# Optimization experiments

Hardware: AMD Instinct MI355X
Metric: run time of the kernel (lower is better)

The kernel has to match this reference:

```python
import jax, jax.numpy as jnp
import numpy as np

N, E, G = 50000, 800000, 500
IN_DIM, EXTRA, HID, HEADS, NCLS = 128, 32, 64, 4, 1
NODE_FEAT2 = HID * HEADS  # 256, input to layer 2
FINAL = NODE_FEAT2 + EXTRA
NODES_PER_GRAPH = N // G  # 100


def gat_layer(h, W, a_l, a_r, b, src, dst, internal_relu):
    # DGL GATConv: fc -> per-head attn logits -> leaky_relu -> edge softmax (over dst) -> weighted sum
    feat = (h @ W).reshape(N, HEADS, HID)            # [N,H,D]
    el = jnp.sum(feat * a_l, axis=-1)                # [N,H]
    er = jnp.sum(feat * a_r, axis=-1)                # [N,H]
    e = jax.nn.leaky_relu(el[src] + er[dst], negative_slope=0.2)  # [E,H]
    m = jax.ops.segment_max(e, dst, num_segments=N)  # [N,H] (stable softmax)
    ex = jnp.exp(e - m[dst])
    denom = jax.ops.segment_sum(ex, dst, num_segments=N)
    alpha = ex / denom[dst]                          # [E,H]
    msg = feat[src] * alpha[:, :, None]              # [E,H,D]
    rst = jax.ops.segment_sum(msg, dst, num_segments=N) + b.reshape(1, HEADS, HID)
    if internal_relu:
        rst = jax.nn.relu(rst)
    return rst


def setup_inputs() -> dict:
    key = jax.random.key(0)
    ks = jax.random.split(key, 20)
    s = 0.05
    inp = {
        "x": jax.random.normal(ks[0], (N, IN_DIM), jnp.float32),
        "desc": jax.random.normal(ks[1], (G, EXTRA), jnp.float32),
        "src": jax.random.randint(ks[2], (E,), 0, N, jnp.int32),
        "dst": jax.random.randint(ks[3], (E,), 0, N, jnp.int32),
        "graph_id": (jnp.arange(N) // NODES_PER_GRAPH).astype(jnp.int32),
        # layer 1 params
        "W1": jax.random.normal(ks[4], (IN_DIM, HEADS * HID), jnp.float32) * s,
        "al1": jax.random.normal(ks[5], (HEADS, HID), jnp.float32) * s,
        "ar1": jax.random.normal(ks[6], (HEADS, HID), jnp.float32) * s,
        "b1": jnp.zeros((HEADS * HID,), jnp.float32),
        # layer 2 params
        "W2": jax.random.normal(ks[7], (NODE_FEAT2, HEADS * HID), jnp.float32) * s,
        "al2": jax.random.normal(ks[8], (HEADS, HID), jnp.float32) * s,
        "ar2": jax.random.normal(ks[9], (HEADS, HID), jnp.float32) * s,
        "b2": jnp.zeros((HEADS * HID,), jnp.float32),
        # MLP head (weights stored [in,out])
        "fc1_w": jax.random.normal(ks[10], (FINAL, HID), jnp.float32) * s,
        "fc1_b": jnp.zeros((HID,), jnp.float32),
        "fc2_w": jax.random.normal(ks[11], (HID, HID // 2), jnp.float32) * s,
        "fc2_b": jnp.zeros((HID // 2,), jnp.float32),
        "out_w": jax.random.normal(ks[12], (HID // 2, NCLS), jnp.float32) * s,
        "out_b": jnp.zeros((NCLS,), jnp.float32),
    }
    return inp


def reference(x, desc, src, dst, graph_id, W1, al1, ar1, b1, W2, al2, ar2, b2,
              fc1_w, fc1_b, fc2_w, fc2_b, out_w, out_b):
    h = gat_layer(x, W1, al1, ar1, b1, src, dst, internal_relu=True)
    h = jax.nn.relu(h.reshape(N, -1))                # flatten heads + outer relu (dropout=0)
    h = gat_layer(h, W2, al2, ar2, b2, src, dst, internal_relu=False)
    h = jax.nn.relu(h.reshape(N, -1))
    # dgl.mean_nodes over batched graph
    hg = jax.ops.segment_sum(h, graph_id, num_segments=G) / float(NODES_PER_GRAPH)  # [G, 256]
    combined = jnp.concatenate([hg, desc], axis=1)   # [G, 288]
    z = jax.nn.relu(combined @ fc1_w + fc1_b)
    z = jax.nn.relu(z @ fc2_w + fc2_b)
    return z @ out_w + out_b                          # [G, 1]
```

## Files before the change

### kernel.cpp

```cpp
#include <hip/hip_runtime.h>
#include <hip/hip_bf16.h>

#define N_NODES 50000
#define N_EDGES 800000
#define N_GRAPHS 500
#define IN_DIM 128
#define EXTRA 32
#define HID 64
#define HEADS 4
#define F2 256
#define NODES_PER_GRAPH 100
#define SCAN_BLOCKS ((N_NODES + 1023) / 1024)

typedef unsigned short u16;
typedef __attribute__((ext_vector_type(8))) short short8;
typedef __attribute__((ext_vector_type(4))) float floatx4;

__device__ __forceinline__ float bf2f(u16 u) {
    union { unsigned int i; float f; } v;
    v.i = ((unsigned int)u) << 16;
    return v.f;
}
__device__ __forceinline__ u16 f2b(float f) {
    __hip_bfloat16 h = __float2bfloat16(f);
    return *reinterpret_cast<u16*>(&h);
}

#define CNT_BLK 3125
#define CVT_BLK 6250
#define RP1_BLK 16
#define RP2_BLK 32
__global__ __launch_bounds__(256) void prep_kernel(const int* __restrict__ dst,
                                                   int* __restrict__ cnt,
                                                   const float* __restrict__ x,
                                                   u16* __restrict__ xb,
                                                   const float* __restrict__ W1,
                                                   u16* __restrict__ BF1,
                                                   const float* __restrict__ W2,
                                                   u16* __restrict__ BF2) {
    int b = blockIdx.x, t = threadIdx.x;
    if (b < CNT_BLK) {
        int e = b * 256 + t;
        if (e < N_EDGES) atomicAdd(&cnt[dst[e]], 1);
    } else if (b < CNT_BLK + CVT_BLK) {
        int i = (b - CNT_BLK) * 256 + t;
        float4 v = reinterpret_cast<const float4*>(x)[i];
        ushort4 o;
        o.x = f2b(v.x); o.y = f2b(v.y); o.z = f2b(v.z); o.w = f2b(v.w);
        reinterpret_cast<ushort4*>(xb)[i] = o;
    } else {
        const float* W;
        u16* BF;
        int chunk;
        if (b < CNT_BLK + CVT_BLK + RP1_BLK) {
            W = W1; BF = BF1; chunk = (b - CNT_BLK - CVT_BLK) * 4 + (t >> 6);
        } else {
            W = W2; BF = BF2; chunk = (b - CNT_BLK - CVT_BLK - RP1_BLK) * 4 + (t >> 6);
        }
        int l = t & 63;
        int kt = chunk >> 4, ct = chunk & 15;
        int col = ct * 16 + (l & 15);
        int k0 = kt * 32 + 8 * (l >> 4);
        u16* p = BF + (size_t)chunk * 512 + l * 8;
#pragma unroll
        for (int j = 0; j < 8; ++j) p[j] = f2b(W[(size_t)(k0 + j) * 256 + col]);
    }
}

__global__ __launch_bounds__(1024) void scan_block_kernel(const int* __restrict__ cnt,
                                                          int* __restrict__ part,
                                                          int* __restrict__ bsum) {
    __shared__ int buf[1024];
    int b = blockIdx.x, t = threadIdx.x;
    int i = b * 1024 + t;
    buf[t] = (i < N_NODES) ? cnt[i] : 0;
    __syncthreads();
    for (int d = 1; d < 1024; d <<= 1) {
        int add = (t >= d) ? buf[t - d] : 0;
        __syncthreads();
        buf[t] += add;
        __syncthreads();
    }
    if (i < N_NODES) part[i] = buf[t];
    if (t == 1023) bsum[b] = buf[t];
}

__global__ __launch_bounds__(1024) void scan_finalize_kernel(const int* __restrict__ part,
                                                             const int* __restrict__ bsum,
                                                             int* __restrict__ offs) {
    __shared__ int sbase;
    int t = threadIdx.x;
    if (t < 64) {
        int v = (t < blockIdx.x) ? bsum[t] : 0;
#pragma unroll
        for (int d = 32; d > 0; d >>= 1) v += __shfl_xor(v, d);
        if (t == 0) sbase = v;
    }
    __syncthreads();
    int i = blockIdx.x * 1024 + t;
    if (i < N_NODES) {
        offs[i + 1] = part[i] + sbase;
        if (i == 0) offs[0] = 0;
    }
}

__global__ void scatter_kernel(const int* __restrict__ src, const int* __restrict__ dst,
                               const int* __restrict__ offs, int* __restrict__ fill,
                               int* __restrict__ csr_src, int* __restrict__ pos_arr) {
    int e = blockIdx.x * blockDim.x + threadIdx.x;
    if (e < N_EDGES) {
        int d = dst[e];
        int pos = offs[d] + atomicAdd(&fill[d], 1);
        csr_src[pos] = src[e];
        pos_arr[e] = pos;
    }
}

__global__ void edge_w_kernel(const int* __restrict__ src, const int* __restrict__ dst,
                              const int* __restrict__ pos_arr,
                              const float* __restrict__ el, const float* __restrict__ er,
                              float* __restrict__ w) {
    int e = blockIdx.x * blockDim.x + threadIdx.x;
    if (e >= N_EDGES) return;
    int s = src[e], d = dst[e], p = pos_arr[e];
    float4 l = *reinterpret_cast<const float4*>(&el[s * 4]);
    float4 r = *reinterpret_cast<const float4*>(&er[d * 4]);
    float4 o; float v;
    v = l.x + r.x; v = (v > 0.f) ? v : 0.2f * v; o.x = __expf(v);
    v = l.y + r.y; v = (v > 0.f) ? v : 0.2f * v; o.y = __expf(v);
    v = l.z + r.z; v = (v > 0.f) ? v : 0.2f * v; o.z = __expf(v);
    v = l.w + r.w; v = (v > 0.f) ? v : 0.2f * v; o.w = __expf(v);
    *reinterpret_cast<float4*>(&w[(size_t)p * 4]) = o;
}

template <int K>
__global__ __launch_bounds__(256) void gemm_mfma_attn_kernel(const u16* __restrict__ A,
                                                             const u16* __restrict__ BF,
                                                             const float* __restrict__ al,
                                                             const float* __restrict__ ar,
                                                             u16* __restrict__ C,
                                                             float* __restrict__ el,
                                                             float* __restrict__ er, int M) {
    __shared__ u16 bstage[8192];
    __shared__ u16 cxpose[4][16 * 68];
    int t = threadIdx.x;
    int wave = t >> 6, lane = t & 63;
    int wr = wave >> 1, wc = wave & 1;
    int l15 = lane & 15, kg = lane >> 4;
    int cb = blockIdx.y;
    int row0 = blockIdx.x * 128 + wr * 64;
    int h = cb * 2 + wc;
    int ct0 = cb * 8 + wc * 4;

    floatx4 acc[4][4];
#pragma unroll
    for (int s = 0; s < 4; ++s)
#pragma unroll
        for (int c = 0; c < 4; ++c) acc[s][c] = (floatx4)0.0f;

    int arow[4];
#pragma unroll
    for (int s = 0; s < 4; ++s) {
        int r = row0 + s * 16 + l15;
        arow[s] = (r < M) ? r : 0;
    }

    int schunk = t >> 4;
    int soff = (t & 15) * 32;

    for (int ks = 0; ks < K / 64; ++ks) {
        __syncthreads();
        {
            int gchunk = (ks * 2 + (schunk >> 3)) * 16 + cb * 8 + (schunk & 7);
            const u16* gp = BF + (size_t)gchunk * 512 + soff;
            u16* lp = bstage + schunk * 512 + soff;
#pragma unroll
            for (int u = 0; u < 4; ++u)
                *reinterpret_cast<short8*>(lp + u * 8) =
                    *reinterpret_cast<const short8*>(gp + u * 8);
        }
        __syncthreads();
#pragma unroll
        for (int ktl = 0; ktl < 2; ++ktl) {
            int kk = (ks * 2 + ktl) * 32 + kg * 8;
            short8 a[4], b[4];
#pragma unroll
            for (int s = 0; s < 4; ++s)
                a[s] = *reinterpret_cast<const short8*>(A + (size_t)arow[s] * K + kk);
#pragma unroll
            for (int c = 0; c < 4; ++c)
                b[c] = *reinterpret_cast<const short8*>(
                           bstage + (ktl * 8 + wc * 4 + c) * 512 + lane * 8);
#pragma unroll
            for (int s = 0; s < 4; ++s)
#pragma unroll
                for (int c = 0; c < 4; ++c)
                    acc[s][c] = __builtin_amdgcn_mfma_f32_16x16x32_bf16(a[s], b[c], acc[s][c], 0, 0, 0);
        }
    }

    floatx4 pls[4], prs[4];
#pragma unroll
    for (int s = 0; s < 4; ++s) { pls[s] = (floatx4)0.0f; prs[s] = (floatx4)0.0f; }
#pragma unroll
    for (int c = 0; c < 4; ++c) {
        float wl = al[(ct0 + c) * 16 + l15];
        float wrr = ar[(ct0 + c) * 16 + l15];
#pragma unroll
        for (int s = 0; s < 4; ++s) {
            pls[s] += acc[s][c] * wl;
            prs[s] += acc[s][c] * wrr;
        }
    }
#pragma unroll
    for (int off = 1; off < 16; off <<= 1) {
#pragma unroll
        for (int s = 0; s < 4; ++s)
#pragma unroll
            for (int j = 0; j < 4; ++j) {
                pls[s][j] += __shfl_xor(pls[s][j], off);
                prs[s][j] += __shfl_xor(prs[s][j], off);
            }
    }
    if (l15 == 0) {
#pragma unroll
        for (int s = 0; s < 4; ++s)
#pragma unroll
            for (int j = 0; j < 4; ++j) {
                int n = row0 + s * 16 + kg * 4 + j;
                if (n < M) { el[n * 4 + h] = pls[s][j]; er[n * 4 + h] = prs[s][j]; }
            }
    }

    u16* cbuf = cxpose[wave];
#pragma unroll
    for (int s = 0; s < 4; ++s) {
#pragma unroll
        for (int c = 0; c < 4; ++c)
#pragma unroll
            for (int j = 0; j < 4; ++j)
                cbuf[(kg * 4 + j) * 68 + c * 16 + l15] = f2b(acc[s][c][j]);
#pragma unroll
        for (int it = 0; it < 2; ++it) {
            int r = (lane >> 3) + it * 8;
            int cg = lane & 7;
            int grow = row0 + s * 16 + r;
            if (grow < M) {
                short8 v = *reinterpret_cast<const short8*>(cbuf + r * 68 + cg * 8);
                *reinterpret_cast<short8*>(C + (size_t)grow * 256 + ct0 * 16 + cg * 8) = v;
            }
        }
    }
}

__global__ __launch_bounds__(256) void gather_kernel(const u16* __restrict__ feat,
                                                     const float* __restrict__ w,
                                                     const int* __restrict__ offs,
                                                     const int* __restrict__ csr_src,
                                                     const float* __restrict__ bias,
                                                     u16* __restrict__ outb) {
    int n = blockIdx.x * 4 + (threadIdx.x >> 6);
    if (n >= N_NODES) return;
    int lane = threadIdx.x & 63;
    int h = lane >> 4;
    const ushort4* feat4 = reinterpret_cast<const ushort4*>(feat);
    int s0 = offs[n], s1 = offs[n + 1];
    float4 acc = make_float4(0.f, 0.f, 0.f, 0.f);
    float den = 0.f;
    int i = s0;
    for (; i + 4 <= s1; i += 4) {
        int n0 = csr_src[i], n1 = csr_src[i + 1], n2 = csr_src[i + 2], n3 = csr_src[i + 3];
        float x0 = w[(size_t)(i + 0) * 4 + h];
        float x1 = w[(size_t)(i + 1) * 4 + h];
        float x2 = w[(size_t)(i + 2) * 4 + h];
        float x3 = w[(size_t)(i + 3) * 4 + h];
        ushort4 f0 = feat4[(size_t)n0 * 64 + lane];
        ushort4 f1 = feat4[(size_t)n1 * 64 + lane];
        ushort4 f2 = feat4[(size_t)n2 * 64 + lane];
        ushort4 f3 = feat4[(size_t)n3 * 64 + lane];
        acc.x = fmaf(x0, bf2f(f0.x), acc.x); acc.y = fmaf(x0, bf2f(f0.y), acc.y);
        acc.z = fmaf(x0, bf2f(f0.z), acc.z); acc.w = fmaf(x0, bf2f(f0.w), acc.w);
        acc.x = fmaf(x1, bf2f(f1.x), acc.x); acc.y = fmaf(x1, bf2f(f1.y), acc.y);
        acc.z = fmaf(x1, bf2f(f1.z), acc.z); acc.w = fmaf(x1, bf2f(f1.w), acc.w);
        acc.x = fmaf(x2, bf2f(f2.x), acc.x); acc.y = fmaf(x2, bf2f(f2.y), acc.y);
        acc.z = fmaf(x2, bf2f(f2.z), acc.z); acc.w = fmaf(x2, bf2f(f2.w), acc.w);
        acc.x = fmaf(x3, bf2f(f3.x), acc.x); acc.y = fmaf(x3, bf2f(f3.y), acc.y);
        acc.z = fmaf(x3, bf2f(f3.z), acc.z); acc.w = fmaf(x3, bf2f(f3.w), acc.w);
        den += (x0 + x1) + (x2 + x3);
    }
    for (; i < s1; ++i) {
        int s = csr_src[i];
        float x = w[(size_t)i * 4 + h];
        ushort4 f = feat4[(size_t)s * 64 + lane];
        acc.x = fmaf(x, bf2f(f.x), acc.x); acc.y = fmaf(x, bf2f(f.y), acc.y);
        acc.z = fmaf(x, bf2f(f.z), acc.z); acc.w = fmaf(x, bf2f(f.w), acc.w);
        den += x;
    }
    float inv = (s1 > s0) ? 1.f / den : 0.f;
    float4 bv = reinterpret_cast<const float4*>(bias)[lane];
    ushort4 o;
    o.x = f2b(fmaxf(fmaf(acc.x, inv, bv.x), 0.f));
    o.y = f2b(fmaxf(fmaf(acc.y, inv, bv.y), 0.f));
    o.z = f2b(fmaxf(fmaf(acc.z, inv, bv.z), 0.f));
    o.w = f2b(fmaxf(fmaf(acc.w, inv, bv.w), 0.f));
    reinterpret_cast<ushort4*>(outb)[(size_t)n * 64 + lane] = o;
}

__global__ __launch_bounds__(256) void head_kernel(const u16* __restrict__ h2,
                                                   const float* __restrict__ desc,
                                                   const float* __restrict__ fc1_w,
                                                   const float* __restrict__ fc1_b,
                                                   const float* __restrict__ fc2_w,
                                                   const float* __restrict__ fc2_b,
                                                   const float* __restrict__ out_w,
                                                   const float* __restrict__ out_b,
                                                   float* __restrict__ out) {
    __shared__ float comb[288];
    __shared__ float z1[64];
    __shared__ float z2[32];
    int g = blockIdx.x, t = threadIdx.x;
    const u16* base = h2 + (size_t)g * NODES_PER_GRAPH * 256;
    float s = 0.f;
    for (int i = 0; i < NODES_PER_GRAPH; ++i) s += bf2f(base[(size_t)i * 256 + t]);
    comb[t] = s * (1.f / NODES_PER_GRAPH);
    if (t < EXTRA) comb[256 + t] = desc[g * EXTRA + t];
    __syncthreads();
    if (t < 64) {
        float a = fc1_b[t];
        for (int i = 0; i < 288; ++i) a += comb[i] * fc1_w[i * 64 + t];
        z1[t] = fmaxf(a, 0.f);
    }
    __syncthreads();
    if (t < 32) {
        float a = fc2_b[t];
        for (int i = 0; i < 64; ++i) a += z1[i] * fc2_w[i * 32 + t];
        z2[t] = fmaxf(a, 0.f);
    }
    __syncthreads();
    if (t == 0) {
        float a = out_b[0];
        for (int i = 0; i < 32; ++i) a += z2[i] * out_w[i];
        out[g] = a;
    }
}

extern "C" void kernel_launch(void* const* d_in, const int* in_sizes, int n_in,
                              void* d_out, int out_size, void* d_ws, size_t ws_size,
                              hipStream_t stream) {
    const float* x     = (const float*)d_in[0];
    const float* desc  = (const float*)d_in[1];
    const int*   src   = (const int*)d_in[2];
    const int*   dst   = (const int*)d_in[3];
    const float* W1    = (const float*)d_in[5];
    const float* al1   = (const float*)d_in[6];
    const float* ar1   = (const float*)d_in[7];
    const float* b1    = (const float*)d_in[8];
    const float* W2    = (const float*)d_in[9];
    const float* al2   = (const float*)d_in[10];
    const float* ar2   = (const float*)d_in[11];
    const float* b2    = (const float*)d_in[12];
    const float* fc1_w = (const float*)d_in[13];
    const float* fc1_b = (const float*)d_in[14];
    const float* fc2_w = (const float*)d_in[15];
    const float* fc2_b = (const float*)d_in[16];
    const float* out_w = (const float*)d_in[17];
    const float* out_b = (const float*)d_in[18];
    float* out = (float*)d_out;

    char* ws = (char*)d_ws;
    size_t off = 0;
    auto alloc = [&](size_t bytes) -> void* {
        void* p = ws + off;
        off = (off + bytes + 255) & ~(size_t)255;
        return p;
    };
    u16*   xb      = (u16*)alloc((size_t)N_NODES * IN_DIM * 2);
    u16*   featb   = (u16*)alloc((size_t)N_NODES * 256 * 2);
    u16*   h1b     = (u16*)alloc((size_t)N_NODES * 256 * 2);
    u16*   h2b     = (u16*)alloc((size_t)N_NODES * 256 * 2);
    u16*   BF1     = (u16*)alloc((size_t)IN_DIM * 256 * 2);
    u16*   BF2     = (u16*)alloc((size_t)F2 * 256 * 2);
    float* el      = (float*)alloc((size_t)N_NODES * 4 * 4);
    float* er      = (float*)alloc((size_t)N_NODES * 4 * 4);
    int*   offs    = (int*)alloc((size_t)(N_NODES + 1) * 4);
    int*   cntfill = (int*)alloc((size_t)2 * N_NODES * 4);
    int*   part    = (int*)alloc((size_t)N_NODES * 4);
    int*   bsum    = (int*)alloc(64 * 4);
    int*   csr_src = (int*)alloc((size_t)N_EDGES * 4);
    int*   pos_arr = (int*)alloc((size_t)N_EDGES * 4);
    float* wbuf    = (float*)alloc((size_t)N_EDGES * 4 * 4);
    int* cnt = cntfill, *fill = cntfill + N_NODES;

    hipMemsetAsync(cntfill, 0, (size_t)2 * N_NODES * 4, stream);
    prep_kernel<<<CNT_BLK + CVT_BLK + RP1_BLK + RP2_BLK, 256, 0, stream>>>(
        dst, cnt, x, xb, W1, BF1, W2, BF2);
    scan_block_kernel<<<SCAN_BLOCKS, 1024, 0, stream>>>(cnt, part, bsum);
    scan_finalize_kernel<<<SCAN_BLOCKS, 1024, 0, stream>>>(part, bsum, offs);
    scatter_kernel<<<(N_EDGES + 255) / 256, 256, 0, stream>>>(src, dst, offs, fill,
                                                              csr_src, pos_arr);

    dim3 gg((N_NODES + 127) / 128, 2);
    int eb = (N_EDGES + 255) / 256;
    gemm_mfma_attn_kernel<IN_DIM><<<gg, 256, 0, stream>>>(xb, BF1, al1, ar1, featb, el, er, N_NODES);
    edge_w_kernel<<<eb, 256, 0, stream>>>(src, dst, pos_arr, el, er, wbuf);
    gather_kernel<<<(N_NODES + 3) / 4, 256, 0, stream>>>(featb, wbuf, offs, csr_src, b1, h1b);
    gemm_mfma_attn_kernel<F2><<<gg, 256, 0, stream>>>(h1b, BF2, al2, ar2, featb, el, er, N_NODES);
    edge_w_kernel<<<eb, 256, 0, stream>>>(src, dst, pos_arr, el, er, wbuf);
    gather_kernel<<<(N_NODES + 3) / 4, 256, 0, stream>>>(featb, wbuf, offs, csr_src, b2, h2b);
    head_kernel<<<N_GRAPHS, 256, 0, stream>>>(h2b, desc, fc1_w, fc1_b, fc2_w, fc2_b,
                                              out_w, out_b, out);
}
```

Measured before the change: 314.5 us.

## Fuse CSR scatter with layer-1 edge weights and widen gather to half-wave per node

The CSR scatter is merged with the first layer's edge-weight computation, so one edge pass writes csr_src, pos_arr and the exp-weights, and a launch plus a reread of src/dst is dropped. The gather kernel now gives each node 32 lanes that each load 8 bf16 values (16-byte loads), fitting 8 nodes per block, and unrolls by 2 with a wave-wide __any loop. The head kernel's mean reduction is split into 4 accumulators. Two half-wave nodes with different degrees now share one loop, which can leave lanes idle, and the unroll drops from 4 to 2.

```diff
diff --git a/kernel.cpp b/kernel.cpp
--- a/kernel.cpp
+++ b/kernel.cpp
@@ -104,16 +104,25 @@
     }
 }
 
-__global__ void scatter_kernel(const int* __restrict__ src, const int* __restrict__ dst,
-                               const int* __restrict__ offs, int* __restrict__ fill,
-                               int* __restrict__ csr_src, int* __restrict__ pos_arr) {
+__global__ void scatter_w_kernel(const int* __restrict__ src, const int* __restrict__ dst,
+                                 const int* __restrict__ offs, int* __restrict__ fill,
+                                 int* __restrict__ csr_src, int* __restrict__ pos_arr,
+                                 const float* __restrict__ el, const float* __restrict__ er,
+                                 float* __restrict__ w) {
     int e = blockIdx.x * blockDim.x + threadIdx.x;
-    if (e < N_EDGES) {
-        int d = dst[e];
-        int pos = offs[d] + atomicAdd(&fill[d], 1);
-        csr_src[pos] = src[e];
-        pos_arr[e] = pos;
-    }
+    if (e >= N_EDGES) return;
+    int s = src[e], d = dst[e];
+    int pos = offs[d] + atomicAdd(&fill[d], 1);
+    csr_src[pos] = s;
+    pos_arr[e] = pos;
+    float4 l = *reinterpret_cast<const float4*>(&el[s * 4]);
+    float4 r = *reinterpret_cast<const float4*>(&er[d * 4]);
+    float4 o; float v;
+    v = l.x + r.x; v = (v > 0.f) ? v : 0.2f * v; o.x = __expf(v);
+    v = l.y + r.y; v = (v > 0.f) ? v : 0.2f * v; o.y = __expf(v);
+    v = l.z + r.z; v = (v > 0.f) ? v : 0.2f * v; o.z = __expf(v);
+    v = l.w + r.w; v = (v > 0.f) ? v : 0.2f * v; o.w = __expf(v);
+    *reinterpret_cast<float4*>(&w[(size_t)pos * 4]) = o;
 }
 
 __global__ void edge_w_kernel(const int* __restrict__ src, const int* __restrict__ dst,
@@ -259,51 +268,49 @@
                                                      const int* __restrict__ csr_src,
                                                      const float* __restrict__ bias,
                                                      u16* __restrict__ outb) {
-    int n = blockIdx.x * 4 + (threadIdx.x >> 6);
-    if (n >= N_NODES) return;
-    int lane = threadIdx.x & 63;
-    int h = lane >> 4;
-    const ushort4* feat4 = reinterpret_cast<const ushort4*>(feat);
-    int s0 = offs[n], s1 = offs[n + 1];
-    float4 acc = make_float4(0.f, 0.f, 0.f, 0.f);
+    int half = threadIdx.x >> 5;
+    int n = blockIdx.x * 8 + half;
+    int l = threadIdx.x & 31;
+    int h = l >> 3;
+    bool valid = n < N_NODES;
+    int s0 = valid ? offs[n] : 0;
+    int s1 = valid ? offs[n + 1] : 0;
+
+    float acc[8] = {0.f, 0.f, 0.f, 0.f, 0.f, 0.f, 0.f, 0.f};
     float den = 0.f;
     int i = s0;
-    for (; i + 4 <= s1; i += 4) {
-        int n0 = csr_src[i], n1 = csr_src[i + 1], n2 = csr_src[i + 2], n3 = csr_src[i + 3];
-        float x0 = w[(size_t)(i + 0) * 4 + h];
-        float x1 = w[(size_t)(i + 1) * 4 + h];
-        float x2 = w[(size_t)(i + 2) * 4 + h];
-        float x3 = w[(size_t)(i + 3) * 4 + h];
-        ushort4 f0 = feat4[(size_t)n0 * 64 + lane];
-        ushort4 f1 = feat4[(size_t)n1 * 64 + lane];
-        ushort4 f2 = feat4[(size_t)n2 * 64 + lane];
-        ushort4 f3 = feat4[(size_t)n3 * 64 + lane];
-        acc.x = fmaf(x0, bf2f(f0.x), acc.x); acc.y = fmaf(x0, bf2f(f0.y), acc.y);
-        acc.z = fmaf(x0, bf2f(f0.z), acc.z); acc.w = fmaf(x0, bf2f(f0.w), acc.w);
-        acc.x = fmaf(x1, bf2f(f1.x), acc.x); acc.y = fmaf(x1, bf2f(f1.y), acc.y);
-        acc.z = fmaf(x1, bf2f(f1.z), acc.z); acc.w = fmaf(x1, bf2f(f1.w), acc.w);
-        acc.x = fmaf(x2, bf2f(f2.x), acc.x); acc.y = fmaf(x2, bf2f(f2.y), acc.y);
-        acc.z = fmaf(x2, bf2f(f2.z), acc.z); acc.w = fmaf(x2, bf2f(f2.w), acc.w);
-        acc.x = fmaf(x3, bf2f(f3.x), acc.x); acc.y = fmaf(x3, bf2f(f3.y), acc.y);
-        acc.z = fmaf(x3, bf2f(f3.z), acc.z); acc.w = fmaf(x3, bf2f(f3.w), acc.w);
-        den += (x0 + x1) + (x2 + x3);
-    }
-    for (; i < s1; ++i) {
-        int s = csr_src[i];
-        float x = w[(size_t)i * 4 + h];
-        ushort4 f = feat4[(size_t)s * 64 + lane];
-        acc.x = fmaf(x, bf2f(f.x), acc.x); acc.y = fmaf(x, bf2f(f.y), acc.y);
-        acc.z = fmaf(x, bf2f(f.z), acc.z); acc.w = fmaf(x, bf2f(f.w), acc.w);
-        den += x;
-    }
-    float inv = (s1 > s0) ? 1.f / den : 0.f;
-    float4 bv = reinterpret_cast<const float4*>(bias)[lane];
-    ushort4 o;
-    o.x = f2b(fmaxf(fmaf(acc.x, inv, bv.x), 0.f));
-    o.y = f2b(fmaxf(fmaf(acc.y, inv, bv.y), 0.f));
-    o.z = f2b(fmaxf(fmaf(acc.z, inv, bv.z), 0.f));
-    o.w = f2b(fmaxf(fmaf(acc.w, inv, bv.w), 0.f));
-    reinterpret_cast<ushort4*>(outb)[(size_t)n * 64 + lane] = o;
+    while (__any(i < s1)) {
+        bool p0 = i < s1, p1 = (i + 1) < s1;
+        float x0 = 0.f, x1 = 0.f;
+        short8 f0 = (short8)0, f1 = (short8)0;
+        if (p0) {
+            int e0 = csr_src[i];
+            x0 = w[(size_t)i * 4 + h];
+            f0 = *reinterpret_cast<const short8*>(feat + (size_t)e0 * 256 + l * 8);
+        }
+        if (p1) {
+            int e1 = csr_src[i + 1];
+            x1 = w[(size_t)(i + 1) * 4 + h];
+            f1 = *reinterpret_cast<const short8*>(feat + (size_t)e1 * 256 + l * 8);
+        }
+#pragma unroll
+        for (int j = 0; j < 8; ++j) acc[j] = fmaf(x0, bf2f((u16)f0[j]), acc[j]);
+#pragma unroll
+        for (int j = 0; j < 8; ++j) acc[j] = fmaf(x1, bf2f((u16)f1[j]), acc[j]);
+        den += x0 + x1;
+        i += 2;
+    }
+    if (valid) {
+        float inv = (s1 > s0) ? 1.f / den : 0.f;
+        float4 bv0 = reinterpret_cast<const float4*>(bias)[l * 2];
+        float4 bv1 = reinterpret_cast<const float4*>(bias)[l * 2 + 1];
+        float bb[8] = {bv0.x, bv0.y, bv0.z, bv0.w, bv1.x, bv1.y, bv1.z, bv1.w};
+        short8 o;
+#pragma unroll
+        for (int j = 0; j < 8; ++j)
+            o[j] = (short)f2b(fmaxf(fmaf(acc[j], inv, bb[j]), 0.f));
+        *reinterpret_cast<short8*>(outb + (size_t)n * 256 + l * 8) = o;
+    }
 }
 
 __global__ __launch_bounds__(256) void head_kernel(const u16* __restrict__ h2,
@@ -320,9 +327,14 @@
     __shared__ float z2[32];
     int g = blockIdx.x, t = threadIdx.x;
     const u16* base = h2 + (size_t)g * NODES_PER_GRAPH * 256;
-    float s = 0.f;
-    for (int i = 0; i < NODES_PER_GRAPH; ++i) s += bf2f(base[(size_t)i * 256 + t]);
-    comb[t] = s * (1.f / NODES_PER_GRAPH);
+    float s0 = 0.f, s1 = 0.f, s2 = 0.f, s3 = 0.f;
+    for (int i = 0; i < NODES_PER_GRAPH; i += 4) {
+        s0 += bf2f(base[(size_t)(i + 0) * 256 + t]);
+        s1 += bf2f(base[(size_t)(i + 1) * 256 + t]);
+        s2 += bf2f(base[(size_t)(i + 2) * 256 + t]);
+        s3 += bf2f(base[(size_t)(i + 3) * 256 + t]);
+    }
+    comb[t] = ((s0 + s1) + (s2 + s3)) * (1.f / NODES_PER_GRAPH);
     if (t < EXTRA) comb[256 + t] = desc[g * EXTRA + t];
     __syncthreads();
     if (t < 64) {
@@ -396,17 +408,17 @@
         dst, cnt, x, xb, W1, BF1, W2, BF2);
     scan_block_kernel<<<SCAN_BLOCKS, 1024, 0, stream>>>(cnt, part, bsum);
     scan_finalize_kernel<<<SCAN_BLOCKS, 1024, 0, stream>>>(part, bsum, offs);
-    scatter_kernel<<<(N_EDGES + 255) / 256, 256, 0, stream>>>(src, dst, offs, fill,
-                                                              csr_src, pos_arr);
 
     dim3 gg((N_NODES + 127) / 128, 2);
     int eb = (N_EDGES + 255) / 256;
+    int ngb = (N_NODES + 7) / 8;
     gemm_mfma_attn_kernel<IN_DIM><<<gg, 256, 0, stream>>>(xb, BF1, al1, ar1, featb, el, er, N_NODES);
-    edge_w_kernel<<<eb, 256, 0, stream>>>(src, dst, pos_arr, el, er, wbuf);
-    gather_kernel<<<(N_NODES + 3) / 4, 256, 0, stream>>>(featb, wbuf, offs, csr_src, b1, h1b);
+    scatter_w_kernel<<<eb, 256, 0, stream>>>(src, dst, offs, fill, csr_src, pos_arr,
+                                             el, er, wbuf);
+    gather_kernel<<<ngb, 256, 0, stream>>>(featb, wbuf, offs, csr_src, b1, h1b);
     gemm_mfma_attn_kernel<F2><<<gg, 256, 0, stream>>>(h1b, BF2, al2, ar2, featb, el, er, N_NODES);
     edge_w_kernel<<<eb, 256, 0, stream>>>(src, dst, pos_arr, el, er, wbuf);
-    gather_kernel<<<(N_NODES + 3) / 4, 256, 0, stream>>>(featb, wbuf, offs, csr_src, b2, h2b);
+    gather_kernel<<<ngb, 256, 0, stream>>>(featb, wbuf, offs, csr_src, b2, h2b);
     head_kernel<<<N_GRAPHS, 256, 0, stream>>>(h2b, desc, fc1_w, fc1_b, fc2_w, fc2_b,
                                               out_w, out_b, out);
 }
```

Measured after the change: 320.9 us. 1.02x slower.

## Fuse CSR scatter with layer-1 edge weights and restage GEMM A tile in LDS

Applied to the files above, without the earlier changes.

The CSR scatter kernel now also computes the layer-1 edge attention weights, which removes one edge pass and one kernel launch. The GEMM is retiled so each block owns 64 rows across all four heads. The A tile is staged in shared memory once and reused by all four waves instead of each wave loading it from global memory, and the full B matrix slice is staged per k-step. The head kernel's per-graph mean loop is also unrolled into four independent accumulators. In exchange the GEMM uses more shared memory per block and has fewer waves per row tile, which may lower occupancy.

```diff
diff --git a/kernel.cpp b/kernel.cpp
--- a/kernel.cpp
+++ b/kernel.cpp
@@ -104,16 +104,25 @@
     }
 }
 
-__global__ void scatter_kernel(const int* __restrict__ src, const int* __restrict__ dst,
-                               const int* __restrict__ offs, int* __restrict__ fill,
-                               int* __restrict__ csr_src, int* __restrict__ pos_arr) {
+__global__ void scatter_w_kernel(const int* __restrict__ src, const int* __restrict__ dst,
+                                 const int* __restrict__ offs, int* __restrict__ fill,
+                                 int* __restrict__ csr_src, int* __restrict__ pos_arr,
+                                 const float* __restrict__ el, const float* __restrict__ er,
+                                 float* __restrict__ w) {
     int e = blockIdx.x * blockDim.x + threadIdx.x;
-    if (e < N_EDGES) {
-        int d = dst[e];
-        int pos = offs[d] + atomicAdd(&fill[d], 1);
-        csr_src[pos] = src[e];
-        pos_arr[e] = pos;
-    }
+    if (e >= N_EDGES) return;
+    int s = src[e], d = dst[e];
+    int pos = offs[d] + atomicAdd(&fill[d], 1);
+    csr_src[pos] = s;
+    pos_arr[e] = pos;
+    float4 l = *reinterpret_cast<const float4*>(&el[s * 4]);
+    float4 r = *reinterpret_cast<const float4*>(&er[d * 4]);
+    float4 o; float v;
+    v = l.x + r.x; v = (v > 0.f) ? v : 0.2f * v; o.x = __expf(v);
+    v = l.y + r.y; v = (v > 0.f) ? v : 0.2f * v; o.y = __expf(v);
+    v = l.z + r.z; v = (v > 0.f) ? v : 0.2f * v; o.z = __expf(v);
+    v = l.w + r.w; v = (v > 0.f) ? v : 0.2f * v; o.w = __expf(v);
+    *reinterpret_cast<float4*>(&w[(size_t)pos * 4]) = o;
 }
 
 __global__ void edge_w_kernel(const int* __restrict__ src, const int* __restrict__ dst,
@@ -141,16 +150,13 @@
                                                              u16* __restrict__ C,
                                                              float* __restrict__ el,
                                                              float* __restrict__ er, int M) {
-    __shared__ u16 bstage[8192];
-    __shared__ u16 cxpose[4][16 * 68];
+    __shared__ u16 astage[64][68];
+    __shared__ u16 bstage[16384];
     int t = threadIdx.x;
     int wave = t >> 6, lane = t & 63;
-    int wr = wave >> 1, wc = wave & 1;
+    int wc = wave;
     int l15 = lane & 15, kg = lane >> 4;
-    int cb = blockIdx.y;
-    int row0 = blockIdx.x * 128 + wr * 64;
-    int h = cb * 2 + wc;
-    int ct0 = cb * 8 + wc * 4;
+    int row0 = blockIdx.x * 64;
 
     floatx4 acc[4][4];
 #pragma unroll
@@ -158,39 +164,38 @@
 #pragma unroll
         for (int c = 0; c < 4; ++c) acc[s][c] = (floatx4)0.0f;
 
-    int arow[4];
-#pragma unroll
-    for (int s = 0; s < 4; ++s) {
-        int r = row0 + s * 16 + l15;
-        arow[s] = (r < M) ? r : 0;
-    }
-
-    int schunk = t >> 4;
-    int soff = (t & 15) * 32;
+    int arow_l = t >> 3;
+    int akoff = (t & 7) * 8;
 
     for (int ks = 0; ks < K / 64; ++ks) {
         __syncthreads();
+#pragma unroll
+        for (int i = 0; i < 2; ++i) {
+            int rl = arow_l + i * 32;
+            int gr = row0 + rl; if (gr >= M) gr = M - 1;
+            *reinterpret_cast<short8*>(&astage[rl][akoff]) =
+                *reinterpret_cast<const short8*>(A + (size_t)gr * K + ks * 64 + akoff);
+        }
         {
-            int gchunk = (ks * 2 + (schunk >> 3)) * 16 + cb * 8 + (schunk & 7);
-            const u16* gp = BF + (size_t)gchunk * 512 + soff;
-            u16* lp = bstage + schunk * 512 + soff;
-#pragma unroll
-            for (int u = 0; u < 4; ++u)
-                *reinterpret_cast<short8*>(lp + u * 8) =
-                    *reinterpret_cast<const short8*>(gp + u * 8);
+            const u16* bp = BF + (size_t)ks * 16384;
+#pragma unroll
+            for (int j = 0; j < 8; ++j) {
+                int idx = (j * 256 + t) * 8;
+                *reinterpret_cast<short8*>(&bstage[idx]) =
+                    *reinterpret_cast<const short8*>(&bp[idx]);
+            }
         }
         __syncthreads();
 #pragma unroll
         for (int ktl = 0; ktl < 2; ++ktl) {
-            int kk = (ks * 2 + ktl) * 32 + kg * 8;
             short8 a[4], b[4];
 #pragma unroll
             for (int s = 0; s < 4; ++s)
-                a[s] = *reinterpret_cast<const short8*>(A + (size_t)arow[s] * K + kk);
+                a[s] = *reinterpret_cast<const short8*>(&astage[s * 16 + l15][ktl * 32 + kg * 8]);
 #pragma unroll
             for (int c = 0; c < 4; ++c)
                 b[c] = *reinterpret_cast<const short8*>(
-                           bstage + (ktl * 8 + wc * 4 + c) * 512 + lane * 8);
+                           &bstage[(ktl * 16 + wc * 4 + c) * 512 + lane * 8]);
 #pragma unroll
             for (int s = 0; s < 4; ++s)
 #pragma unroll
@@ -199,6 +204,7 @@
         }
     }
 
+    int ct0 = wc * 4;
     floatx4 pls[4], prs[4];
 #pragma unroll
     for (int s = 0; s < 4; ++s) { pls[s] = (floatx4)0.0f; prs[s] = (floatx4)0.0f; }
@@ -228,11 +234,12 @@
 #pragma unroll
             for (int j = 0; j < 4; ++j) {
                 int n = row0 + s * 16 + kg * 4 + j;
-                if (n < M) { el[n * 4 + h] = pls[s][j]; er[n * 4 + h] = prs[s][j]; }
+                if (n < M) { el[n * 4 + wc] = pls[s][j]; er[n * 4 + wc] = prs[s][j]; }
             }
     }
 
-    u16* cbuf = cxpose[wave];
+    __syncthreads();
+    u16* cbuf = &astage[0][0] + wave * 1088;
 #pragma unroll
     for (int s = 0; s < 4; ++s) {
 #pragma unroll
@@ -247,7 +254,7 @@
             int grow = row0 + s * 16 + r;
             if (grow < M) {
                 short8 v = *reinterpret_cast<const short8*>(cbuf + r * 68 + cg * 8);
-                *reinterpret_cast<short8*>(C + (size_t)grow * 256 + ct0 * 16 + cg * 8) = v;
+                *reinterpret_cast<short8*>(C + (size_t)grow * 256 + wc * 64 + cg * 8) = v;
             }
         }
     }
@@ -320,9 +327,14 @@
     __shared__ float z2[32];
     int g = blockIdx.x, t = threadIdx.x;
     const u16* base = h2 + (size_t)g * NODES_PER_GRAPH * 256;
-    float s = 0.f;
-    for (int i = 0; i < NODES_PER_GRAPH; ++i) s += bf2f(base[(size_t)i * 256 + t]);
-    comb[t] = s * (1.f / NODES_PER_GRAPH);
+    float s0 = 0.f, s1 = 0.f, s2 = 0.f, s3 = 0.f;
+    for (int i = 0; i < NODES_PER_GRAPH; i += 4) {
+        s0 += bf2f(base[(size_t)(i + 0) * 256 + t]);
+        s1 += bf2f(base[(size_t)(i + 1) * 256 + t]);
+        s2 += bf2f(base[(size_t)(i + 2) * 256 + t]);
+        s3 += bf2f(base[(size_t)(i + 3) * 256 + t]);
+    }
+    comb[t] = ((s0 + s1) + (s2 + s3)) * (1.f / NODES_PER_GRAPH);
     if (t < EXTRA) comb[256 + t] = desc[g * EXTRA + t];
     __syncthreads();
     if (t < 64) {
@@ -396,17 +408,17 @@
         dst, cnt, x, xb, W1, BF1, W2, BF2);
     scan_block_kernel<<<SCAN_BLOCKS, 1024, 0, stream>>>(cnt, part, bsum);
     scan_finalize_kernel<<<SCAN_BLOCKS, 1024, 0, stream>>>(part, bsum, offs);
-    scatter_kernel<<<(N_EDGES + 255) / 256, 256, 0, stream>>>(src, dst, offs, fill,
-                                                              csr_src, pos_arr);
-
-    dim3 gg((N_NODES + 127) / 128, 2);
+
+    int gb = (N_NODES + 63) / 64;
     int eb = (N_EDGES + 255) / 256;
-    gemm_mfma_attn_kernel<IN_DIM><<<gg, 256, 0, stream>>>(xb, BF1, al1, ar1, featb, el, er, N_NODES);
+    int ngb = (N_NODES + 3) / 4;
+    gemm_mfma_attn_kernel<IN_DIM><<<gb, 256, 0, stream>>>(xb, BF1, al1, ar1, featb, el, er, N_NODES);
+    scatter_w_kernel<<<eb, 256, 0, stream>>>(src, dst, offs, fill, csr_src, pos_arr,
+                                             el, er, wbuf);
+    gather_kernel<<<ngb, 256, 0, stream>>>(featb, wbuf, offs, csr_src, b1, h1b);
+    gemm_mfma_attn_kernel<F2><<<gb, 256, 0, stream>>>(h1b, BF2, al2, ar2, featb, el, er, N_NODES);
     edge_w_kernel<<<eb, 256, 0, stream>>>(src, dst, pos_arr, el, er, wbuf);
-    gather_kernel<<<(N_NODES + 3) / 4, 256, 0, stream>>>(featb, wbuf, offs, csr_src, b1, h1b);
-    gemm_mfma_attn_kernel<F2><<<gg, 256, 0, stream>>>(h1b, BF2, al2, ar2, featb, el, er, N_NODES);
-    edge_w_kernel<<<eb, 256, 0, stream>>>(src, dst, pos_arr, el, er, wbuf);
-    gather_kernel<<<(N_NODES + 3) / 4, 256, 0, stream>>>(featb, wbuf, offs, csr_src, b2, h2b);
+    gather_kernel<<<ngb, 256, 0, stream>>>(featb, wbuf, offs, csr_src, b2, h2b);
     head_kernel<<<N_GRAPHS, 256, 0, stream>>>(h2b, desc, fc1_w, fc1_b, fc2_w, fc2_b,
                                               out_w, out_b, out);
 }
```

Result: faster. 289.3 us (-8.0%).
